# Performance work log

Hardware: AMD Instinct MI355X
Metric: run time of the kernel (lower is better)

Reference implementation:

```python
import jax, jax.numpy as jnp
import numpy as np
from jax import lax

VOCAB_SIZE = 13
E = 13          # embedding_dim == len(VOCAB)
H = 1024        # weights_dim (LSTM hidden)
HL = 512        # hidden_layer_dim (MLP)
OUT = 2
T = 16384       # sequence length


def setup_inputs() -> dict:
    key = jax.random.key(0)
    ks = jax.random.split(key, 12)
    s_ih = 1.0 / np.sqrt(H)  # PyTorch LSTMCell default init scale
    inp = {
        "x": jax.random.normal(ks[0], (T, E), dtype=jnp.float32),
        "h0": jax.random.normal(ks[1], (1, H), dtype=jnp.float32) * np.sqrt(2.0 / (1 + H)),
        "c0": jax.random.normal(ks[2], (1, H), dtype=jnp.float32) * np.sqrt(2.0 / (1 + H)),
        "W_ih": jax.random.uniform(ks[3], (4 * H, E), jnp.float32, -s_ih, s_ih),
        "W_hh": jax.random.uniform(ks[4], (4 * H, H), jnp.float32, -s_ih, s_ih),
        "b_ih": jax.random.uniform(ks[5], (4 * H,), jnp.float32, -s_ih, s_ih),
        "b_hh": jax.random.uniform(ks[6], (4 * H,), jnp.float32, -s_ih, s_ih),
        "W1": jax.random.uniform(ks[7], (HL, H), jnp.float32, -1.0 / np.sqrt(H), 1.0 / np.sqrt(H)),
        "b1": jax.random.uniform(ks[8], (HL,), jnp.float32, -1.0 / np.sqrt(H), 1.0 / np.sqrt(H)),
        "W2": jax.random.uniform(ks[9], (OUT, HL), jnp.float32, -1.0 / np.sqrt(HL), 1.0 / np.sqrt(HL)),
        "b2": jax.random.uniform(ks[10], (OUT,), jnp.float32, -1.0 / np.sqrt(HL), 1.0 / np.sqrt(HL)),
    }
    return inp


def reference(x, h0, c0, W_ih, W_hh, b_ih, b_hh, W1, b1, W2, b2):
    # x: [T, E] (batch dim of the original view is 1, folded away)
    # Precompute input-to-gate projections for all timesteps (same math, one GEMM).
    xg = x @ W_ih.T + b_ih  # [T, 4H]

    def step(carry, xg_t):
        h, c = carry  # [1, H] each
        gates = xg_t + h @ W_hh.T + b_hh  # [1, 4H]
        i, f, g, o = jnp.split(gates, 4, axis=-1)
        c = jax.nn.sigmoid(f) * c + jax.nn.sigmoid(i) * jnp.tanh(g)
        h = jax.nn.sigmoid(o) * jnp.tanh(c)
        return (h, c), None

    (h, c), _ = lax.scan(step, (h0, c0), xg[:, None, :])
    out = jnp.tanh(h @ W1.T + b1) @ W2.T + b2  # [1, 2]
    return out
```

## Files before the change

### kernel.cpp

```cpp
#include <hip/hip_runtime.h>
#include <cstdint>
#include <cstddef>

#define NWG 64
#define NTHR 512
#define TSTEPS 16384
#define HDIM 1024
#define EDIM 13
#define HLDIM 512

typedef unsigned long long ull;

__global__ void k_init(const float* __restrict__ h0, ull* __restrict__ hrec,
                       ull* __restrict__ urec) {
  int i = threadIdx.x;
  hrec[i] = (ull)__float_as_uint(h0[i]);
  hrec[HDIM + i] = 0ull;
  hrec[2 * HDIM + i] = 0ull;
  hrec[3 * HDIM + i] = 0ull;
  if (i < HLDIM) urec[i] = 0ull;
}

__global__ __launch_bounds__(NTHR)
__attribute__((amdgpu_waves_per_eu(2, 2))) void k_main(
    const float* __restrict__ x, const float* __restrict__ c0,
    const float* __restrict__ Wih, const float* __restrict__ Whh,
    const float* __restrict__ bih, const float* __restrict__ bhh,
    const float* __restrict__ W1, const float* __restrict__ b1,
    const float* __restrict__ W2, const float* __restrict__ b2,
    float* __restrict__ out, ull* hrec, ull* urec) {
  const int w = blockIdx.x;
  const int tid = threadIdx.x;
  const int sub = tid & 7;
  const int row = tid >> 3;
  const int wave = tid >> 6;
  const int lane = tid & 63;
  const int g = row & 3;
  const int lu = row >> 2;
  const int grow = g * HDIM + w * 16 + lu;

  __shared__ float4 lds_h4[2][HDIM / 4];
  __shared__ float lds_x[2][16];
  __shared__ float lds_wih[64][17];
  __shared__ float lds_bsum[64];
  __shared__ float lds_r0[8], lds_r1[8];
  float* lds_hf = (float*)lds_h4;

  float4 wreg[32];
  const float4* wrow = (const float4*)(Whh + (size_t)grow * HDIM) + sub * 32;
#pragma unroll
  for (int i = 0; i < 32; ++i) wreg[i] = wrow[(i + sub) & 31];
#pragma unroll
  for (int i = 0; i < 32; ++i)
    asm volatile("" : "+v"(wreg[i].x), "+v"(wreg[i].y), "+v"(wreg[i].z),
                     "+v"(wreg[i].w));

  if (tid < 64) {
    int g2 = tid & 3, lu2 = tid >> 2;
    int gr2 = g2 * HDIM + w * 16 + lu2;
#pragma unroll
    for (int e = 0; e < EDIM; ++e) lds_wih[tid][e] = Wih[gr2 * EDIM + e];
    lds_bsum[tid] = bih[gr2] + bhh[gr2];
  }
  float cst = c0[w * 16 + 2 * wave + (lane >> 5)];
  __syncthreads();

  const float gsc = (g == 2) ? 2.f : 1.f;

  for (int t = 1; t <= TSTEPS; ++t) {
    const int lp = (t - 1) & 1;
    float xv = 0.f;
    if (tid < EDIM) xv = x[(size_t)(t - 1) * EDIM + tid];

    const ull* src = hrec + (size_t)((t - 1) & 3) * HDIM;
    const unsigned want = (unsigned)(t - 1);
    ull v0 = __hip_atomic_load(&src[tid], __ATOMIC_RELAXED,
                               __HIP_MEMORY_SCOPE_AGENT);
    ull v1 = __hip_atomic_load(&src[tid + NTHR], __ATOMIC_RELAXED,
                               __HIP_MEMORY_SCOPE_AGENT);
    for (;;) {
      bool b0 = (unsigned)(v0 >> 32) == want;
      bool b1 = (unsigned)(v1 >> 32) == want;
      if (b0 && b1) break;
      if (!b0)
        v0 = __hip_atomic_load(&src[tid], __ATOMIC_RELAXED,
                               __HIP_MEMORY_SCOPE_AGENT);
      if (!b1)
        v1 = __hip_atomic_load(&src[tid + NTHR], __ATOMIC_RELAXED,
                               __HIP_MEMORY_SCOPE_AGENT);
    }
    lds_hf[lp * HDIM + tid] = __uint_as_float((unsigned)v0);
    lds_hf[lp * HDIM + tid + NTHR] = __uint_as_float((unsigned)v1);
    if (tid < EDIM) lds_x[lp][tid] = xv;
    __syncthreads();

    float acc = lds_wih[row][sub] * lds_x[lp][sub];
    if (sub < EDIM - 8) acc += lds_wih[row][sub + 8] * lds_x[lp][sub + 8];
    if (sub == 0) acc += lds_bsum[row];
#pragma unroll
    for (int i = 0; i < 32; ++i) {
      float4 hv = lds_h4[lp][sub * 32 + ((i + sub) & 31)];
      float4 wv = wreg[i];
      acc += wv.x * hv.x;
      acc += wv.y * hv.y;
      acc += wv.z * hv.z;
      acc += wv.w * hv.w;
    }
    acc += __shfl_xor(acc, 1);
    acc += __shfl_xor(acc, 2);
    acc += __shfl_xor(acc, 4);

    float e = __expf(-gsc * acc);
    float y = 1.f / (1.f + e);
    float act = (g == 2) ? 2.f * y - 1.f : y;

    int base = lane & 32;
    float ai = __shfl(act, base + 0);
    float af = __shfl(act, base + 8);
    float ag = __shfl(act, base + 16);
    float ao = __shfl(act, base + 24);
    if ((lane & 31) == 0) {
      cst = af * cst + ai * ag;
      float e2 = __expf(-2.f * cst);
      float hn = ao * (2.f / (1.f + e2) - 1.f);
      ull pk = ((ull)(unsigned)t << 32) | (ull)__float_as_uint(hn);
      __hip_atomic_store(&hrec[(size_t)(t & 3) * HDIM + w * 16 + 2 * wave +
                               (lane >> 5)],
                         pk, __ATOMIC_RELAXED, __HIP_MEMORY_SCOPE_AGENT);
    }
  }

  {
    const unsigned want = (unsigned)TSTEPS;
    ull v0 = __hip_atomic_load(&hrec[tid], __ATOMIC_RELAXED,
                               __HIP_MEMORY_SCOPE_AGENT);
    ull v1 = __hip_atomic_load(&hrec[tid + NTHR], __ATOMIC_RELAXED,
                               __HIP_MEMORY_SCOPE_AGENT);
    for (;;) {
      bool b0 = (unsigned)(v0 >> 32) == want;
      bool b1 = (unsigned)(v1 >> 32) == want;
      if (b0 && b1) break;
      if (!b0)
        v0 = __hip_atomic_load(&hrec[tid], __ATOMIC_RELAXED,
                               __HIP_MEMORY_SCOPE_AGENT);
      if (!b1)
        v1 = __hip_atomic_load(&hrec[tid + NTHR], __ATOMIC_RELAXED,
                               __HIP_MEMORY_SCOPE_AGENT);
    }
    lds_hf[tid] = __uint_as_float((unsigned)v0);
    lds_hf[tid + NTHR] = __uint_as_float((unsigned)v1);
  }
  __syncthreads();
  {
    int r1 = 8 * w + wave;
    const float* w1p = W1 + (size_t)r1 * HDIM + lane * 16;
    float acc1 = 0.f;
#pragma unroll
    for (int i = 0; i < 16; ++i) acc1 += w1p[i] * lds_hf[lane * 16 + i];
#pragma unroll
    for (int m = 1; m < 64; m <<= 1) acc1 += __shfl_xor(acc1, m);
    if (lane == 0) {
      float e2 = __expf(-2.f * (acc1 + b1[r1]));
      float u = 2.f / (1.f + e2) - 1.f;
      ull pk = (1ull << 32) | (ull)__float_as_uint(u);
      __hip_atomic_store(&urec[r1], pk, __ATOMIC_RELAXED,
                         __HIP_MEMORY_SCOPE_AGENT);
    }
  }

  if (w == 0) {
    ull uv = __hip_atomic_load(&urec[tid], __ATOMIC_RELAXED,
                               __HIP_MEMORY_SCOPE_AGENT);
    while ((unsigned)(uv >> 32) != 1u)
      uv = __hip_atomic_load(&urec[tid], __ATOMIC_RELAXED,
                             __HIP_MEMORY_SCOPE_AGENT);
    float u = __uint_as_float((unsigned)uv);
    float p0 = W2[tid] * u;
    float p1 = W2[HLDIM + tid] * u;
#pragma unroll
    for (int m = 1; m < 64; m <<= 1) {
      p0 += __shfl_xor(p0, m);
      p1 += __shfl_xor(p1, m);
    }
    if (lane == 0) {
      lds_r0[wave] = p0;
      lds_r1[wave] = p1;
    }
    __syncthreads();
    if (tid == 0) {
      float o0 = b2[0], o1 = b2[1];
#pragma unroll
      for (int k = 0; k < 8; ++k) {
        o0 += lds_r0[k];
        o1 += lds_r1[k];
      }
      out[0] = o0;
      out[1] = o1;
    }
  }
}

extern "C" void kernel_launch(void* const* d_in, const int* in_sizes, int n_in,
                              void* d_out, int out_size, void* d_ws,
                              size_t ws_size, hipStream_t stream) {
  const float* x = (const float*)d_in[0];
  const float* h0 = (const float*)d_in[1];
  const float* c0 = (const float*)d_in[2];
  const float* Wih = (const float*)d_in[3];
  const float* Whh = (const float*)d_in[4];
  const float* bih = (const float*)d_in[5];
  const float* bhh = (const float*)d_in[6];
  const float* W1 = (const float*)d_in[7];
  const float* b1 = (const float*)d_in[8];
  const float* W2 = (const float*)d_in[9];
  const float* b2 = (const float*)d_in[10];
  float* out = (float*)d_out;

  ull* hrec = (ull*)d_ws;
  ull* urec = (ull*)((char*)d_ws + 4 * HDIM * sizeof(ull));

  k_init<<<1, 1024, 0, stream>>>(h0, hrec, urec);
  k_main<<<NWG, NTHR, 0, stream>>>(x, c0, Wih, Whh, bih, bhh, W1, b1, W2, b2,
                                   out, hrec, urec);
}
```

Baseline: 49.31 ms.

## Double threads per workgroup, halve per-thread weight slice, split accumulators

Raises the workgroup size from 512 to 1024 threads. Each gate row is now split across 16 lanes holding 16 float4 weights each, down from 8 lanes holding 32, so the per-step dot product chain is shorter and the dependency is broken over four accumulators. Each wave now owns one hidden unit, and each thread polls a single h record instead of two. A large unused LDS pad, kept alive by a dummy kernel argument, appears meant to force one workgroup per CU. The costs are an extra shuffle reduction stage and more waves contending at the per-step barrier.

```diff
diff --git a/kernel.cpp b/kernel.cpp
--- a/kernel.cpp
+++ b/kernel.cpp
@@ -3,7 +3,7 @@
 #include <cstddef>
 
 #define NWG 64
-#define NTHR 512
+#define NTHR 1024
 #define TSTEPS 16384
 #define HDIM 1024
 #define EDIM 13
@@ -22,36 +22,37 @@
 }
 
 __global__ __launch_bounds__(NTHR)
-__attribute__((amdgpu_waves_per_eu(2, 2))) void k_main(
+__attribute__((amdgpu_waves_per_eu(4, 4))) void k_main(
     const float* __restrict__ x, const float* __restrict__ c0,
     const float* __restrict__ Wih, const float* __restrict__ Whh,
     const float* __restrict__ bih, const float* __restrict__ bhh,
     const float* __restrict__ W1, const float* __restrict__ b1,
     const float* __restrict__ W2, const float* __restrict__ b2,
-    float* __restrict__ out, ull* hrec, ull* urec) {
+    float* __restrict__ out, ull* hrec, ull* urec, int never) {
   const int w = blockIdx.x;
   const int tid = threadIdx.x;
-  const int sub = tid & 7;
-  const int row = tid >> 3;
+  const int sub = tid & 15;
+  const int row = tid >> 4;
   const int wave = tid >> 6;
   const int lane = tid & 63;
   const int g = row & 3;
-  const int lu = row >> 2;
-  const int grow = g * HDIM + w * 16 + lu;
+  const int grow = g * HDIM + w * 16 + (row >> 2);
 
   __shared__ float4 lds_h4[2][HDIM / 4];
   __shared__ float lds_x[2][16];
   __shared__ float lds_wih[64][17];
   __shared__ float lds_bsum[64];
   __shared__ float lds_r0[8], lds_r1[8];
+  __shared__ float lds_pad[17408];
   float* lds_hf = (float*)lds_h4;
-
-  float4 wreg[32];
-  const float4* wrow = (const float4*)(Whh + (size_t)grow * HDIM) + sub * 32;
-#pragma unroll
-  for (int i = 0; i < 32; ++i) wreg[i] = wrow[(i + sub) & 31];
-#pragma unroll
-  for (int i = 0; i < 32; ++i)
+  if (never) ((volatile float*)lds_pad)[0] = 1.f;
+
+  float4 wreg[16];
+  const float4* wrow4 = (const float4*)(Whh + (size_t)grow * HDIM);
+#pragma unroll
+  for (int i = 0; i < 16; ++i) wreg[i] = wrow4[sub * 16 + ((i + sub) & 15)];
+#pragma unroll
+  for (int i = 0; i < 16; ++i)
     asm volatile("" : "+v"(wreg[i].x), "+v"(wreg[i].y), "+v"(wreg[i].z),
                      "+v"(wreg[i].w));
 
@@ -62,7 +63,7 @@
     for (int e = 0; e < EDIM; ++e) lds_wih[tid][e] = Wih[gr2 * EDIM + e];
     lds_bsum[tid] = bih[gr2] + bhh[gr2];
   }
-  float cst = c0[w * 16 + 2 * wave + (lane >> 5)];
+  float cst = c0[w * 16 + wave];
   __syncthreads();
 
   const float gsc = (g == 2) ? 2.f : 1.f;
@@ -72,91 +73,72 @@
     float xv = 0.f;
     if (tid < EDIM) xv = x[(size_t)(t - 1) * EDIM + tid];
 
-    const ull* src = hrec + (size_t)((t - 1) & 3) * HDIM;
+    const ull* rec = hrec + (size_t)((t - 1) & 3) * HDIM + tid;
     const unsigned want = (unsigned)(t - 1);
-    ull v0 = __hip_atomic_load(&src[tid], __ATOMIC_RELAXED,
-                               __HIP_MEMORY_SCOPE_AGENT);
-    ull v1 = __hip_atomic_load(&src[tid + NTHR], __ATOMIC_RELAXED,
-                               __HIP_MEMORY_SCOPE_AGENT);
-    for (;;) {
-      bool b0 = (unsigned)(v0 >> 32) == want;
-      bool b1 = (unsigned)(v1 >> 32) == want;
-      if (b0 && b1) break;
-      if (!b0)
-        v0 = __hip_atomic_load(&src[tid], __ATOMIC_RELAXED,
-                               __HIP_MEMORY_SCOPE_AGENT);
-      if (!b1)
-        v1 = __hip_atomic_load(&src[tid + NTHR], __ATOMIC_RELAXED,
-                               __HIP_MEMORY_SCOPE_AGENT);
-    }
-    lds_hf[lp * HDIM + tid] = __uint_as_float((unsigned)v0);
-    lds_hf[lp * HDIM + tid + NTHR] = __uint_as_float((unsigned)v1);
+    ull v = __hip_atomic_load(rec, __ATOMIC_RELAXED, __HIP_MEMORY_SCOPE_AGENT);
+    while ((unsigned)(v >> 32) != want)
+      v = __hip_atomic_load(rec, __ATOMIC_RELAXED, __HIP_MEMORY_SCOPE_AGENT);
+    lds_hf[lp * HDIM + tid] = __uint_as_float((unsigned)v);
     if (tid < EDIM) lds_x[lp][tid] = xv;
     __syncthreads();
 
-    float acc = lds_wih[row][sub] * lds_x[lp][sub];
-    if (sub < EDIM - 8) acc += lds_wih[row][sub + 8] * lds_x[lp][sub + 8];
-    if (sub == 0) acc += lds_bsum[row];
-#pragma unroll
-    for (int i = 0; i < 32; ++i) {
-      float4 hv = lds_h4[lp][sub * 32 + ((i + sub) & 31)];
+    float acc0 = 0.f, acc1 = 0.f, acc2 = 0.f, acc3 = 0.f;
+    if (sub < EDIM) acc0 = lds_wih[row][sub] * lds_x[lp][sub];
+    if (sub == 0) acc1 = lds_bsum[row];
+#pragma unroll
+    for (int i = 0; i < 16; ++i) {
+      float4 hv = lds_h4[lp][sub * 16 + ((i + sub) & 15)];
       float4 wv = wreg[i];
-      acc += wv.x * hv.x;
-      acc += wv.y * hv.y;
-      acc += wv.z * hv.z;
-      acc += wv.w * hv.w;
-    }
+      float pr = wv.x * hv.x + wv.y * hv.y;
+      float ps = wv.z * hv.z + wv.w * hv.w;
+      if ((i & 3) == 0) { acc0 += pr; acc1 += ps; }
+      else if ((i & 3) == 1) { acc2 += pr; acc3 += ps; }
+      else if ((i & 3) == 2) { acc0 += pr; acc1 += ps; }
+      else { acc2 += pr; acc3 += ps; }
+    }
+    float acc = (acc0 + acc1) + (acc2 + acc3);
     acc += __shfl_xor(acc, 1);
     acc += __shfl_xor(acc, 2);
     acc += __shfl_xor(acc, 4);
+    acc += __shfl_xor(acc, 8);
 
     float e = __expf(-gsc * acc);
     float y = 1.f / (1.f + e);
     float act = (g == 2) ? 2.f * y - 1.f : y;
 
-    int base = lane & 32;
-    float ai = __shfl(act, base + 0);
-    float af = __shfl(act, base + 8);
-    float ag = __shfl(act, base + 16);
-    float ao = __shfl(act, base + 24);
-    if ((lane & 31) == 0) {
+    float ai = __shfl(act, 0);
+    float af = __shfl(act, 16);
+    float ag = __shfl(act, 32);
+    float ao = __shfl(act, 48);
+    if (lane == 0) {
       cst = af * cst + ai * ag;
       float e2 = __expf(-2.f * cst);
       float hn = ao * (2.f / (1.f + e2) - 1.f);
       ull pk = ((ull)(unsigned)t << 32) | (ull)__float_as_uint(hn);
-      __hip_atomic_store(&hrec[(size_t)(t & 3) * HDIM + w * 16 + 2 * wave +
-                               (lane >> 5)],
-                         pk, __ATOMIC_RELAXED, __HIP_MEMORY_SCOPE_AGENT);
+      __hip_atomic_store(&hrec[(size_t)(t & 3) * HDIM + w * 16 + wave], pk,
+                         __ATOMIC_RELAXED, __HIP_MEMORY_SCOPE_AGENT);
     }
   }
 
   {
     const unsigned want = (unsigned)TSTEPS;
-    ull v0 = __hip_atomic_load(&hrec[tid], __ATOMIC_RELAXED,
-                               __HIP_MEMORY_SCOPE_AGENT);
-    ull v1 = __hip_atomic_load(&hrec[tid + NTHR], __ATOMIC_RELAXED,
-                               __HIP_MEMORY_SCOPE_AGENT);
-    for (;;) {
-      bool b0 = (unsigned)(v0 >> 32) == want;
-      bool b1 = (unsigned)(v1 >> 32) == want;
-      if (b0 && b1) break;
-      if (!b0)
-        v0 = __hip_atomic_load(&hrec[tid], __ATOMIC_RELAXED,
-                               __HIP_MEMORY_SCOPE_AGENT);
-      if (!b1)
-        v1 = __hip_atomic_load(&hrec[tid + NTHR], __ATOMIC_RELAXED,
-                               __HIP_MEMORY_SCOPE_AGENT);
-    }
-    lds_hf[tid] = __uint_as_float((unsigned)v0);
-    lds_hf[tid + NTHR] = __uint_as_float((unsigned)v1);
+    const ull* rec = hrec + tid;
+    ull v = __hip_atomic_load(rec, __ATOMIC_RELAXED, __HIP_MEMORY_SCOPE_AGENT);
+    while ((unsigned)(v >> 32) != want)
+      v = __hip_atomic_load(rec, __ATOMIC_RELAXED, __HIP_MEMORY_SCOPE_AGENT);
+    lds_hf[tid] = __uint_as_float((unsigned)v);
   }
   __syncthreads();
-  {
+  if (wave < 8) {
     int r1 = 8 * w + wave;
     const float* w1p = W1 + (size_t)r1 * HDIM + lane * 16;
-    float acc1 = 0.f;
-#pragma unroll
-    for (int i = 0; i < 16; ++i) acc1 += w1p[i] * lds_hf[lane * 16 + i];
+    float a0 = 0.f, a1 = 0.f;
+#pragma unroll
+    for (int i = 0; i < 16; i += 2) {
+      a0 += w1p[i] * lds_hf[lane * 16 + i];
+      a1 += w1p[i + 1] * lds_hf[lane * 16 + i + 1];
+    }
+    float acc1 = a0 + a1;
 #pragma unroll
     for (int m = 1; m < 64; m <<= 1) acc1 += __shfl_xor(acc1, m);
     if (lane == 0) {
@@ -169,20 +151,23 @@
   }
 
   if (w == 0) {
-    ull uv = __hip_atomic_load(&urec[tid], __ATOMIC_RELAXED,
+    float p0 = 0.f, p1 = 0.f;
+    if (tid < HLDIM) {
+      ull uv = __hip_atomic_load(&urec[tid], __ATOMIC_RELAXED,
+                                 __HIP_MEMORY_SCOPE_AGENT);
+      while ((unsigned)(uv >> 32) != 1u)
+        uv = __hip_atomic_load(&urec[tid], __ATOMIC_RELAXED,
                                __HIP_MEMORY_SCOPE_AGENT);
-    while ((unsigned)(uv >> 32) != 1u)
-      uv = __hip_atomic_load(&urec[tid], __ATOMIC_RELAXED,
-                             __HIP_MEMORY_SCOPE_AGENT);
-    float u = __uint_as_float((unsigned)uv);
-    float p0 = W2[tid] * u;
-    float p1 = W2[HLDIM + tid] * u;
+      float u = __uint_as_float((unsigned)uv);
+      p0 = W2[tid] * u;
+      p1 = W2[HLDIM + tid] * u;
+    }
 #pragma unroll
     for (int m = 1; m < 64; m <<= 1) {
       p0 += __shfl_xor(p0, m);
       p1 += __shfl_xor(p1, m);
     }
-    if (lane == 0) {
+    if (lane == 0 && wave < 8) {
       lds_r0[wave] = p0;
       lds_r1[wave] = p1;
     }
@@ -219,7 +204,7 @@
   ull* hrec = (ull*)d_ws;
   ull* urec = (ull*)((char*)d_ws + 4 * HDIM * sizeof(ull));
 
-  k_init<<<1, 1024, 0, stream>>>(h0, hrec, urec);
+  k_init<<<1, NTHR, 0, stream>>>(h0, hrec, urec);
   k_main<<<NWG, NTHR, 0, stream>>>(x, c0, Wih, Whh, bih, bhh, W1, b1, W2, b2,
-                                   out, hrec, urec);
+                                   out, hrec, urec, 0);
 }
```

Result: slower. 67.02 ms (+35.9%).
